# Kernel optimization log

Measured on AMD Instinct MI355X. Metric: run time of the kernel, lower is better.

Reference implementation:

```python
import jax, jax.numpy as jnp
import numpy as np

K = 121          # kernel_size
C = 3            # channels
PAD = (K - 1) // 2  # 60, replicate padding so output matches input spatial size


def setup_inputs() -> dict:
    key = jax.random.key(0)
    k1, k2 = jax.random.split(key)
    x = jax.random.normal(k1, (8, C, 512, 512), dtype=jnp.float32)
    sigma = jax.random.uniform(k2, (), dtype=jnp.float32)
    return {"x": x, "sigma": sigma}


def _gaussian_kernel(sigma):
    # sigma -> sigma*8 + 16, variance = sigma**2 (as in torch forward)
    s = sigma * 8.0 + 16.0
    variance = s * s
    coord = jnp.arange(K, dtype=jnp.float32) - (K - 1) / 2.0  # centered coords
    diff = -(coord[:, None] ** 2 + coord[None, :] ** 2)       # [K,K], -((x-m)^2+(y-m)^2)
    kern = jnp.exp(diff / (2.0 * variance))
    # the 1/(2*pi*variance) prefactor cancels under normalization
    kern = kern / jnp.sum(kern)
    return kern


def reference(x, sigma):
    kern = _gaussian_kernel(sigma)
    # depthwise weights: [out_ch=C, in_ch/groups=1, K, K]
    w = jnp.broadcast_to(kern[None, None, :, :], (C, 1, K, K))
    # replicate padding (torch 'replicate' == jnp 'edge')
    xp = jnp.pad(x, ((0, 0), (0, 0), (PAD, PAD), (PAD, PAD)), mode="edge")
    out = jax.lax.conv_general_dilated(
        xp, w,
        window_strides=(1, 1),
        padding="VALID",
        dimension_numbers=("NCHW", "OIHW", "NCHW"),
        feature_group_count=C,
    )
    return out
```

## Files before the change

kernel.cpp:

```cpp
#include <hip/hip_runtime.h>


#define HH   512
#define WW   512
#define PLANE (512 * 512)
#define NIMG 24
#define RAD  60

__device__ __forceinline__ void make_weights(const float* __restrict__ sigma,
                                             float* __restrict__ wlds, int tid) {
    const float s = sigma[0] * 8.0f + 16.0f;
    const float inv2v = 1.0f / (2.0f * s * s);
    float sum = 0.0f;
    #pragma unroll
    for (int k = 0; k <= 120; ++k) {
        const float c = (float)k - 60.0f;
        sum += __expf(-c * c * inv2v);
    }
    if (tid < 128) {
        float g = 0.0f;
        if (tid < 121) {
            const float c = (float)tid - 60.0f;
            g = __expf(-c * c * inv2v);
        }
        wlds[tid] = g / sum;
    }
}

#define V_OCT(CUR, NXT, KO)                                               \
    { *(float4*)&wq[0] = *(const float4*)&wlds[(KO) * 8];                 \
      *(float4*)&wq[4] = *(const float4*)&wlds[(KO) * 8 + 4];             \
      _Pragma("unroll")                                                   \
      for (int ki = 0; ki < 8; ++ki) {                                    \
          NXT[ki] = sm4[(r0 + ((KO) + 1) * 8 + ki) * 8 + tx];             \
          const float wk = wq[ki];                                        \
          _Pragma("unroll")                                               \
          for (int j = 0; j < 8; ++j) {                                   \
              const int idx = ki + j;                                     \
              const float4 v = (idx < 8) ? CUR[idx] : NXT[idx - 8];       \
              acc[j].x += wk * v.x; acc[j].y += wk * v.y;                 \
              acc[j].z += wk * v.z; acc[j].w += wk * v.w;                 \
          }                                                               \
      }                                                                   \
    }

__global__ __launch_bounds__(256, 3) void blur_v(
        const float* __restrict__ x, const float* __restrict__ sigma,
        float* __restrict__ tmp) {
    __shared__ float sm[384 * 32];
    __shared__ float wlds[128];
    const int tid = threadIdx.x;
    const int w0  = blockIdx.x * 32;
    const int h0  = blockIdx.y * 256;
    const float* __restrict__ src = x + (size_t)blockIdx.z * PLANE;

    {
        const int fc = (tid & 7) * 4;
        int r = tid >> 3;
        #pragma unroll
        for (int it = 0; it < 12; ++it, r += 32) {
            int gr = h0 - RAD + r;
            gr = gr < 0 ? 0 : (gr > HH - 1 ? HH - 1 : gr);
            *(float4*)&sm[r * 32 + fc] =
                *(const float4*)&src[(size_t)gr * WW + w0 + fc];
        }
    }
    make_weights(sigma, wlds, tid);
    __syncthreads();

    const int tx = tid & 7;
    const int r0 = (tid >> 3) * 8;
    const float4* __restrict__ sm4 = (const float4*)sm;

    float4 acc[8];
    #pragma unroll
    for (int j = 0; j < 8; ++j) acc[j] = make_float4(0.f, 0.f, 0.f, 0.f);

    float4 wa[8], wb[8];
    float  wq[8];
    #pragma unroll
    for (int m = 0; m < 8; ++m) wa[m] = sm4[(r0 + m) * 8 + tx];

    #pragma unroll 1
    for (int ko = 0; ko < 16; ko += 2) {
        V_OCT(wa, wb, ko)
        V_OCT(wb, wa, ko + 1)
    }

    float* __restrict__ dst = tmp + (size_t)blockIdx.z * PLANE;
    #pragma unroll
    for (int j = 0; j < 8; ++j)
        *(float4*)&dst[(size_t)(h0 + r0 + j) * WW + w0 + tx * 4] = acc[j];
}

#define HPG_ROW 972

#define LOADG(DST, G)                                                     \
    { *(float4*)&DST[0] = *(const float4*)&bs[(G) * 12];                  \
      *(float4*)&DST[4] = *(const float4*)&bs[(G) * 12 + 4]; }

#define H_OCT(W0, W1, W2, W3, KO)                                         \
    { LOADG(W3, (KO) + 3)                                                 \
      *(float4*)&wq[0] = *(const float4*)&wlds[(KO) * 8];                 \
      *(float4*)&wq[4] = *(const float4*)&wlds[(KO) * 8 + 4];             \
      _Pragma("unroll")                                                   \
      for (int ki = 0; ki < 8; ++ki) {                                    \
          const float wk = wq[ki];                                        \
          _Pragma("unroll")                                               \
          for (int j = 0; j < 16; ++j) {                                  \
              const int idx = ki + j;                                     \
              const float v = (idx < 8) ? W0[idx]                         \
                            : (idx < 16) ? W1[idx - 8] : W2[idx - 16];    \
              acc[j] += wk * v;                                           \
          }                                                               \
      }                                                                   \
    }

__global__ __launch_bounds__(256, 4) void blur_h(
        const float* __restrict__ tmp, const float* __restrict__ sigma,
        float* __restrict__ out) {
    __shared__ float sm[8 * HPG_ROW];
    __shared__ float wlds[128];
    const int tid = threadIdx.x;
    const int h0  = blockIdx.x * 8;
    const float* __restrict__ src = tmp + (size_t)blockIdx.y * PLANE;

    #pragma unroll
    for (int it = 0; it < 3; ++it) {
        const int c = tid + it * 256;
        if (c < 648) {
            int gc = c - RAD;
            gc = gc < 0 ? 0 : (gc > WW - 1 ? WW - 1 : gc);
            const int la = ((c >> 3) * 12) + (c & 7);
            #pragma unroll
            for (int r = 0; r < 8; ++r)
                sm[r * HPG_ROW + la] = src[(size_t)(h0 + r) * WW + gc];
        }
    }
    make_weights(sigma, wlds, tid);
    __syncthreads();

    const int r    = tid >> 5;
    const int L    = tid & 31;
    const float* __restrict__ bs = sm + r * HPG_ROW + L * 24;

    float w0[8], w1[8], w2[8], w3[8], wq[8];
    float acc[16];
    #pragma unroll
    for (int j = 0; j < 16; ++j) acc[j] = 0.0f;

    LOADG(w0, 0)
    LOADG(w1, 1)
    LOADG(w2, 2)

    #pragma unroll 1
    for (int ko = 0; ko < 16; ko += 4) {
        H_OCT(w0, w1, w2, w3, ko)
        H_OCT(w1, w2, w3, w0, ko + 1)
        H_OCT(w2, w3, w0, w1, ko + 2)
        H_OCT(w3, w0, w1, w2, ko + 3)
    }

    float* __restrict__ dst = out + (size_t)blockIdx.y * PLANE
                                  + (size_t)(h0 + r) * WW + L * 16;
    *(float4*)(dst)      = make_float4(acc[0],  acc[1],  acc[2],  acc[3]);
    *(float4*)(dst + 4)  = make_float4(acc[4],  acc[5],  acc[6],  acc[7]);
    *(float4*)(dst + 8)  = make_float4(acc[8],  acc[9],  acc[10], acc[11]);
    *(float4*)(dst + 12) = make_float4(acc[12], acc[13], acc[14], acc[15]);
}

extern "C" void kernel_launch(void* const* d_in, const int* in_sizes, int n_in,
                              void* d_out, int out_size, void* d_ws, size_t ws_size,
                              hipStream_t stream) {
    const float* x     = (const float*)d_in[0];
    const float* sigma = (const float*)d_in[1];
    float* out = (float*)d_out;
    float* tmp = (float*)d_ws;

    blur_v<<<dim3(WW / 32, HH / 256, NIMG), dim3(256), 0, stream>>>(x, sigma, tmp);
    blur_h<<<dim3(HH / 8, NIMG), dim3(256), 0, stream>>>(tmp, sigma, out);
}
```

Before: 119.8 us.

## Pre-pad intermediate rows and use direct global-to-LDS loads in vertical pass

The vertical pass now writes its output into a wider intermediate buffer (648 columns per row) whose left and right 60-column borders are filled with replicated edge values by the edge blocks. The horizontal pass can then load whole rows with unclamped float4 reads instead of per-element clamped scalar loads. The vertical pass's tile loads also switch to the global_load_lds builtin, which writes straight into shared memory without going through registers. This needs a larger workspace, and the edge blocks do extra border writes.

```diff
diff --git a/kernel.cpp b/kernel.cpp
--- a/kernel.cpp
+++ b/kernel.cpp
@@ -1,11 +1,13 @@
 #include <hip/hip_runtime.h>
 
 
-#define HH   512
-#define WW   512
+#define HH    512
+#define WW    512
 #define PLANE (512 * 512)
-#define NIMG 24
-#define RAD  60
+#define NIMG  24
+#define RAD   60
+#define TROW  648
+#define TPLANE (512 * TROW)
 
 __device__ __forceinline__ void make_weights(const float* __restrict__ sigma,
                                              float* __restrict__ wlds, int tid) {
@@ -55,14 +57,19 @@
     const float* __restrict__ src = x + (size_t)blockIdx.z * PLANE;
 
     {
-        const int fc = (tid & 7) * 4;
+        const int fc   = (tid & 7) * 4;
+        const int wave = tid >> 6;
         int r = tid >> 3;
         #pragma unroll
         for (int it = 0; it < 12; ++it, r += 32) {
             int gr = h0 - RAD + r;
             gr = gr < 0 ? 0 : (gr > HH - 1 ? HH - 1 : gr);
-            *(float4*)&sm[r * 32 + fc] =
-                *(const float4*)&src[(size_t)gr * WW + w0 + fc];
+            const float* gp = &src[(size_t)gr * WW + w0 + fc];
+            float* lp = &sm[1024 * it + 256 * wave];
+            __builtin_amdgcn_global_load_lds(
+                (const __attribute__((address_space(1))) unsigned int*)gp,
+                (__attribute__((address_space(3))) unsigned int*)lp,
+                16, 0, 0);
         }
     }
     make_weights(sigma, wlds, tid);
@@ -87,10 +94,31 @@
         V_OCT(wb, wa, ko + 1)
     }
 
-    float* __restrict__ dst = tmp + (size_t)blockIdx.z * PLANE;
+    float* __restrict__ dst = tmp + (size_t)blockIdx.z * TPLANE;
     #pragma unroll
     for (int j = 0; j < 8; ++j)
-        *(float4*)&dst[(size_t)(h0 + r0 + j) * WW + w0 + tx * 4] = acc[j];
+        *(float4*)&dst[(size_t)(h0 + r0 + j) * TROW + 60 + w0 + tx * 4] = acc[j];
+
+    if (blockIdx.x == 0 && tx == 0) {
+        #pragma unroll
+        for (int j = 0; j < 8; ++j) {
+            const float v = acc[j].x;
+            const float4 q = make_float4(v, v, v, v);
+            float* p = dst + (size_t)(h0 + r0 + j) * TROW;
+            #pragma unroll
+            for (int t = 0; t < 15; ++t) ((float4*)p)[t] = q;
+        }
+    }
+    if (blockIdx.x == (WW / 32) - 1 && tx == 7) {
+        #pragma unroll
+        for (int j = 0; j < 8; ++j) {
+            const float v = acc[j].w;
+            const float4 q = make_float4(v, v, v, v);
+            float* p = dst + (size_t)(h0 + r0 + j) * TROW + 572;
+            #pragma unroll
+            for (int t = 0; t < 19; ++t) ((float4*)p)[t] = q;
+        }
+    }
 }
 
 #define HPG_ROW 972
@@ -123,25 +151,20 @@
     __shared__ float wlds[128];
     const int tid = threadIdx.x;
     const int h0  = blockIdx.x * 8;
-    const float* __restrict__ src = tmp + (size_t)blockIdx.y * PLANE;
-
-    #pragma unroll
-    for (int it = 0; it < 3; ++it) {
-        const int c = tid + it * 256;
-        if (c < 648) {
-            int gc = c - RAD;
-            gc = gc < 0 ? 0 : (gc > WW - 1 ? WW - 1 : gc);
-            const int la = ((c >> 3) * 12) + (c & 7);
-            #pragma unroll
-            for (int r = 0; r < 8; ++r)
-                sm[r * HPG_ROW + la] = src[(size_t)(h0 + r) * WW + gc];
-        }
+    const float* __restrict__ src = tmp + (size_t)blockIdx.y * TPLANE;
+
+    for (int i = tid; i < 8 * 162; i += 256) {
+        const int r = i / 162;
+        const int s = i - r * 162;
+        const int c = s * 4;
+        const float4 v = *(const float4*)&src[(size_t)(h0 + r) * TROW + c];
+        *(float4*)&sm[r * HPG_ROW + (c >> 3) * 12 + (c & 7)] = v;
     }
     make_weights(sigma, wlds, tid);
     __syncthreads();
 
-    const int r    = tid >> 5;
-    const int L    = tid & 31;
+    const int r = tid >> 5;
+    const int L = tid & 31;
     const float* __restrict__ bs = sm + r * HPG_ROW + L * 24;
 
     float w0[8], w1[8], w2[8], w3[8], wq[8];
```

Measured after the change: 129.8 us. +8.3%, slower.

## Fuse vertical and horizontal blur passes into one kernel via LDS

Applied to the files above, without the earlier changes.

Merges the separable vertical and horizontal Gaussian passes into a single kernel. Each block computes the vertical blur for 8 full-width rows directly from global memory, stores them in LDS with replicate padding filled in-place, then runs the horizontal pass. This removes the intermediate buffer round trip and one launch, at the cost of each block re-reading 128 input rows (heavy L2 reliance) and narrower float2 vertical loads with less reuse.

```diff
diff --git a/kernel.cpp b/kernel.cpp
--- a/kernel.cpp
+++ b/kernel.cpp
@@ -1,11 +1,11 @@
 #include <hip/hip_runtime.h>
 
 
-#define HH   512
-#define WW   512
-#define PLANE (512 * 512)
-#define NIMG 24
-#define RAD  60
+#define HH      512
+#define WW      512
+#define PLANE   (512 * 512)
+#define NIMG    24
+#define HPG_ROW 972
 
 __device__ __forceinline__ void make_weights(const float* __restrict__ sigma,
                                              float* __restrict__ wlds, int tid) {
@@ -32,68 +32,18 @@
       *(float4*)&wq[4] = *(const float4*)&wlds[(KO) * 8 + 4];             \
       _Pragma("unroll")                                                   \
       for (int ki = 0; ki < 8; ++ki) {                                    \
-          NXT[ki] = sm4[(r0 + ((KO) + 1) * 8 + ki) * 8 + tx];             \
+          int rr = r0 - 52 + (KO) * 8 + ki;                               \
+          rr = rr < 0 ? 0 : (rr > HH - 1 ? HH - 1 : rr);                  \
+          NXT[ki] = *(const float2*)&src[(size_t)rr * WW];                \
           const float wk = wq[ki];                                        \
           _Pragma("unroll")                                               \
           for (int j = 0; j < 8; ++j) {                                   \
               const int idx = ki + j;                                     \
-              const float4 v = (idx < 8) ? CUR[idx] : NXT[idx - 8];       \
-              acc[j].x += wk * v.x; acc[j].y += wk * v.y;                 \
-              acc[j].z += wk * v.z; acc[j].w += wk * v.w;                 \
+              const float2 v = (idx < 8) ? CUR[idx] : NXT[idx - 8];       \
+              vac[j].x += wk * v.x; vac[j].y += wk * v.y;                 \
           }                                                               \
       }                                                                   \
     }
-
-__global__ __launch_bounds__(256, 3) void blur_v(
-        const float* __restrict__ x, const float* __restrict__ sigma,
-        float* __restrict__ tmp) {
-    __shared__ float sm[384 * 32];
-    __shared__ float wlds[128];
-    const int tid = threadIdx.x;
-    const int w0  = blockIdx.x * 32;
-    const int h0  = blockIdx.y * 256;
-    const float* __restrict__ src = x + (size_t)blockIdx.z * PLANE;
-
-    {
-        const int fc = (tid & 7) * 4;
-        int r = tid >> 3;
-        #pragma unroll
-        for (int it = 0; it < 12; ++it, r += 32) {
-            int gr = h0 - RAD + r;
-            gr = gr < 0 ? 0 : (gr > HH - 1 ? HH - 1 : gr);
-            *(float4*)&sm[r * 32 + fc] =
-                *(const float4*)&src[(size_t)gr * WW + w0 + fc];
-        }
-    }
-    make_weights(sigma, wlds, tid);
-    __syncthreads();
-
-    const int tx = tid & 7;
-    const int r0 = (tid >> 3) * 8;
-    const float4* __restrict__ sm4 = (const float4*)sm;
-
-    float4 acc[8];
-    #pragma unroll
-    for (int j = 0; j < 8; ++j) acc[j] = make_float4(0.f, 0.f, 0.f, 0.f);
-
-    float4 wa[8], wb[8];
-    float  wq[8];
-    #pragma unroll
-    for (int m = 0; m < 8; ++m) wa[m] = sm4[(r0 + m) * 8 + tx];
-
-    #pragma unroll 1
-    for (int ko = 0; ko < 16; ko += 2) {
-        V_OCT(wa, wb, ko)
-        V_OCT(wb, wa, ko + 1)
-    }
-
-    float* __restrict__ dst = tmp + (size_t)blockIdx.z * PLANE;
-    #pragma unroll
-    for (int j = 0; j < 8; ++j)
-        *(float4*)&dst[(size_t)(h0 + r0 + j) * WW + w0 + tx * 4] = acc[j];
-}
-
-#define HPG_ROW 972
 
 #define LOADG(DST, G)                                                     \
     { *(float4*)&DST[0] = *(const float4*)&bs[(G) * 12];                  \
@@ -116,35 +66,60 @@
       }                                                                   \
     }
 
-__global__ __launch_bounds__(256, 4) void blur_h(
-        const float* __restrict__ tmp, const float* __restrict__ sigma,
+__global__ __launch_bounds__(256, 4) void blur_fused(
+        const float* __restrict__ x, const float* __restrict__ sigma,
         float* __restrict__ out) {
     __shared__ float sm[8 * HPG_ROW];
     __shared__ float wlds[128];
     const int tid = threadIdx.x;
-    const int h0  = blockIdx.x * 8;
-    const float* __restrict__ src = tmp + (size_t)blockIdx.y * PLANE;
+    const int r0  = blockIdx.x * 8;
+    const int c0  = tid * 2;
+    const float* __restrict__ src = x + (size_t)blockIdx.y * PLANE + c0;
 
+    float2 wa[8], wb[8], vac[8];
+    float  wq[8];
     #pragma unroll
-    for (int it = 0; it < 3; ++it) {
-        const int c = tid + it * 256;
-        if (c < 648) {
-            int gc = c - RAD;
-            gc = gc < 0 ? 0 : (gc > WW - 1 ? WW - 1 : gc);
-            const int la = ((c >> 3) * 12) + (c & 7);
-            #pragma unroll
-            for (int r = 0; r < 8; ++r)
-                sm[r * HPG_ROW + la] = src[(size_t)(h0 + r) * WW + gc];
-        }
+    for (int m = 0; m < 8; ++m) {
+        int rr = r0 - 60 + m;
+        rr = rr < 0 ? 0 : rr;
+        wa[m] = *(const float2*)&src[(size_t)rr * WW];
     }
     make_weights(sigma, wlds, tid);
+    #pragma unroll
+    for (int j = 0; j < 8; ++j) vac[j] = make_float2(0.f, 0.f);
     __syncthreads();
 
-    const int r    = tid >> 5;
-    const int L    = tid & 31;
+    #pragma unroll 1
+    for (int ko = 0; ko < 16; ko += 2) {
+        V_OCT(wa, wb, ko)
+        V_OCT(wb, wa, ko + 1)
+    }
+
+    {
+        const int p  = c0 + 60;
+        const int la = (p >> 3) * 12 + (p & 7);
+        #pragma unroll
+        for (int j = 0; j < 8; ++j)
+            *(float2*)&sm[j * HPG_ROW + la] = vac[j];
+    }
+    __syncthreads();
+
+    if (tid < 136) {
+        const int p    = (tid < 60) ? tid : 512 + tid;
+        const int dsta = (p >> 3) * 12 + (p & 7);
+        const int srca = (tid < 60) ? (7 * 12 + 4)
+                                    : (71 * 12 + 3);
+        #pragma unroll
+        for (int r = 0; r < 8; ++r)
+            sm[r * HPG_ROW + dsta] = sm[r * HPG_ROW + srca];
+    }
+    __syncthreads();
+
+    const int r = tid >> 5;
+    const int L = tid & 31;
     const float* __restrict__ bs = sm + r * HPG_ROW + L * 24;
 
-    float w0[8], w1[8], w2[8], w3[8], wq[8];
+    float w0[8], w1[8], w2[8], w3[8];
     float acc[16];
     #pragma unroll
     for (int j = 0; j < 16; ++j) acc[j] = 0.0f;
@@ -162,7 +137,7 @@
     }
 
     float* __restrict__ dst = out + (size_t)blockIdx.y * PLANE
-                                  + (size_t)(h0 + r) * WW + L * 16;
+                                  + (size_t)(r0 + r) * WW + L * 16;
     *(float4*)(dst)      = make_float4(acc[0],  acc[1],  acc[2],  acc[3]);
     *(float4*)(dst + 4)  = make_float4(acc[4],  acc[5],  acc[6],  acc[7]);
     *(float4*)(dst + 8)  = make_float4(acc[8],  acc[9],  acc[10], acc[11]);
@@ -175,8 +150,5 @@
     const float* x     = (const float*)d_in[0];
     const float* sigma = (const float*)d_in[1];
     float* out = (float*)d_out;
-    float* tmp = (float*)d_ws;
-
-    blur_v<<<dim3(WW / 32, HH / 256, NIMG), dim3(256), 0, stream>>>(x, sigma, tmp);
-    blur_h<<<dim3(HH / 8, NIMG), dim3(256), 0, stream>>>(tmp, sigma, out);
+    blur_fused<<<dim3(HH / 8, NIMG), dim3(256), 0, stream>>>(x, sigma, out);
 }
```

Result: slower. 130.1 us (+8.6%).
